# Kernel optimization log

Hardware: AMD Instinct MI355X
Metric: run time of the kernel (lower is better)

The kernel has to match this reference:

```python
import jax, jax.numpy as jnp
import numpy as np

N_EMBD = 1024
N_HEAD = 16
HEAD = N_EMBD // N_HEAD
D_FF = 4 * N_EMBD
B, T = 2, 2048


def setup_inputs() -> dict:
    key = jax.random.key(0)
    ks = jax.random.split(key, 12)
    s = 0.02
    return {
        "x": jax.random.normal(ks[0], (B, T, N_EMBD), jnp.float32),
        "Wq": jax.random.normal(ks[1], (N_EMBD, N_EMBD), jnp.float32) * s,
        "bq": jnp.zeros((N_EMBD,), jnp.float32),
        "Wk": jax.random.normal(ks[2], (N_EMBD, N_EMBD), jnp.float32) * s,
        "bk": jnp.zeros((N_EMBD,), jnp.float32),
        "Wv": jax.random.normal(ks[3], (N_EMBD, N_EMBD), jnp.float32) * s,
        "bv": jnp.zeros((N_EMBD,), jnp.float32),
        "Wo": jax.random.normal(ks[4], (N_EMBD, N_EMBD), jnp.float32) * s,
        "bo": jnp.zeros((N_EMBD,), jnp.float32),
        "W1": jax.random.normal(ks[5], (N_EMBD, D_FF), jnp.float32) * s,
        "b1": jnp.zeros((D_FF,), jnp.float32),
        "W2": jax.random.normal(ks[6], (D_FF, N_EMBD), jnp.float32) * s,
        "b2": jnp.zeros((N_EMBD,), jnp.float32),
        "g1": jnp.ones((N_EMBD,), jnp.float32),
        "be1": jnp.zeros((N_EMBD,), jnp.float32),
        "g2": jnp.ones((N_EMBD,), jnp.float32),
        "be2": jnp.zeros((N_EMBD,), jnp.float32),
    }


def _layernorm(x, g, b, eps=1e-3):
    # keras LayerNormalization default epsilon=1e-3
    mu = jnp.mean(x, axis=-1, keepdims=True)
    var = jnp.mean(jnp.square(x - mu), axis=-1, keepdims=True)
    return (x - mu) * jax.lax.rsqrt(var + eps) * g + b


def _attention(h, Wq, bq, Wk, bk, Wv, bv, Wo, bo):
    b, t, _ = h.shape
    q = (h @ Wq + bq).reshape(b, t, N_HEAD, HEAD)
    k = (h @ Wk + bk).reshape(b, t, N_HEAD, HEAD)
    v = (h @ Wv + bv).reshape(b, t, N_HEAD, HEAD)
    scores = jnp.einsum("bthd,bshd->bhts", q, k) / jnp.sqrt(jnp.float32(HEAD))
    causal = jnp.tril(jnp.ones((t, t), bool))
    scores = jnp.where(causal, scores, -jnp.inf)
    w = jax.nn.softmax(scores, axis=-1)  # dropout is identity in eval
    ctx = jnp.einsum("bhts,bshd->bthd", w, v).reshape(b, t, N_EMBD)
    return ctx @ Wo + bo


def reference(x, Wq, bq, Wk, bk, Wv, bv, Wo, bo, W1, b1, W2, b2, g1, be1, g2, be2):
    x = x + _attention(_layernorm(x, g1, be1), Wq, bq, Wk, bk, Wv, bv, Wo, bo)
    h = _layernorm(x, g2, be2)
    ff = jax.nn.relu(h @ W1 + b1) @ W2 + b2
    return x + ff
```

## Files before the change

### kernel.cpp

```cpp
#include <hip/hip_runtime.h>

typedef __bf16 bf16;
typedef __attribute__((ext_vector_type(8))) __bf16 bf16x8;
typedef __attribute__((ext_vector_type(4))) __bf16 bf16x4;
typedef __attribute__((ext_vector_type(4))) float f32x4;

#define MFMA16(A, B, C) __builtin_amdgcn_mfma_f32_16x16x32_bf16(A, B, C, 0, 0, 0)

#define GLOAD16(gp, lp)                                          \
  __builtin_amdgcn_global_load_lds(                              \
      (const __attribute__((address_space(1))) void*)(gp),       \
      (__attribute__((address_space(3))) void*)(lp), 16, 0, 0)

__device__ __forceinline__ float fexp2(float x) {
#if __has_builtin(__builtin_amdgcn_exp2f)
  return __builtin_amdgcn_exp2f(x);
#else
  float r;
  asm("v_exp_f32 %0, %1" : "=v"(r) : "v"(x));
  return r;
#endif
}

#define QSCL 0.18033688011112042f

__global__ __launch_bounds__(256) void transpose_all_kernel(
    const float* __restrict__ w0, const float* __restrict__ w1,
    const float* __restrict__ w2, const float* __restrict__ w3,
    bf16* __restrict__ out4,
    const float* __restrict__ W1, bf16* __restrict__ w1t,
    const float* __restrict__ W2, bf16* __restrict__ w2t)
{
  __shared__ float tile[32][33];
  const int bid = blockIdx.x;
  const float* in;
  bf16* out;
  int K, N, kt, nt;
  if (bid < 4096) {
    const float* srcs[4] = {w0, w1, w2, w3};
    in = srcs[bid >> 10];
    out = out4 + (size_t)(bid >> 10) * 1024 * 1024;
    K = 1024; N = 1024;
    const int t = bid & 1023;
    nt = (t & 31) * 32; kt = (t >> 5) * 32;
  } else if (bid < 8192) {
    in = W1; out = w1t; K = 1024; N = 4096;
    const int t = bid - 4096;
    nt = (t & 127) * 32; kt = (t >> 7) * 32;
  } else {
    in = W2; out = w2t; K = 4096; N = 1024;
    const int t = bid - 8192;
    nt = (t & 31) * 32; kt = (t >> 5) * 32;
  }
  const int tx = threadIdx.x, ty = threadIdx.y;
#pragma unroll
  for (int j = 0; j < 4; ++j)
    tile[ty + j * 8][tx] = in[(size_t)(kt + ty + j * 8) * N + nt + tx];
  __syncthreads();
#pragma unroll
  for (int j = 0; j < 4; ++j)
    out[(size_t)(nt + ty + j * 8) * K + kt + tx] = (bf16)tile[tx][ty + j * 8];
}

__global__ __launch_bounds__(256) void ln_kernel(
    const float* __restrict__ in, const float* __restrict__ gamma,
    const float* __restrict__ beta, bf16* __restrict__ out)
{
  const int row = blockIdx.x;
  const int t = threadIdx.x;
  const float4 v = ((const float4*)(in + (size_t)row * 1024))[t];
  float s = v.x + v.y + v.z + v.w;
  float sq = v.x * v.x + v.y * v.y + v.z * v.z + v.w * v.w;
#pragma unroll
  for (int m = 1; m < 64; m <<= 1) {
    s += __shfl_xor(s, m);
    sq += __shfl_xor(sq, m);
  }
  __shared__ float ssum[4], ssq[4];
  const int w = t >> 6;
  if ((t & 63) == 0) { ssum[w] = s; ssq[w] = sq; }
  __syncthreads();
  s = ssum[0] + ssum[1] + ssum[2] + ssum[3];
  sq = ssq[0] + ssq[1] + ssq[2] + ssq[3];
  const float mu = s * (1.0f / 1024.0f);
  const float var = sq * (1.0f / 1024.0f) - mu * mu;
  const float rs = rsqrtf(var + 1e-3f);
  const float4 g = ((const float4*)gamma)[t];
  const float4 b = ((const float4*)beta)[t];
  bf16x4 o;
  o[0] = (bf16)((v.x - mu) * rs * g.x + b.x);
  o[1] = (bf16)((v.y - mu) * rs * g.y + b.y);
  o[2] = (bf16)((v.z - mu) * rs * g.z + b.z);
  o[3] = (bf16)((v.w - mu) * rs * g.w + b.w);
  *(bf16x4*)(out + (size_t)row * 1024 + t * 4) = o;
}

__global__ __launch_bounds__(256) void ln_b_kernel(
    const bf16* __restrict__ in, const float* __restrict__ gamma,
    const float* __restrict__ beta, bf16* __restrict__ out)
{
  const int row = blockIdx.x;
  const int t = threadIdx.x;
  const bf16x4 vb = *(const bf16x4*)(in + (size_t)row * 1024 + t * 4);
  float v0 = (float)vb[0], v1 = (float)vb[1], v2 = (float)vb[2], v3 = (float)vb[3];
  float s = v0 + v1 + v2 + v3;
  float sq = v0 * v0 + v1 * v1 + v2 * v2 + v3 * v3;
#pragma unroll
  for (int m = 1; m < 64; m <<= 1) {
    s += __shfl_xor(s, m);
    sq += __shfl_xor(sq, m);
  }
  __shared__ float ssum[4], ssq[4];
  const int w = t >> 6;
  if ((t & 63) == 0) { ssum[w] = s; ssq[w] = sq; }
  __syncthreads();
  s = ssum[0] + ssum[1] + ssum[2] + ssum[3];
  sq = ssq[0] + ssq[1] + ssq[2] + ssq[3];
  const float mu = s * (1.0f / 1024.0f);
  const float var = sq * (1.0f / 1024.0f) - mu * mu;
  const float rs = rsqrtf(var + 1e-3f);
  const float4 g = ((const float4*)gamma)[t];
  const float4 b = ((const float4*)beta)[t];
  bf16x4 o;
  o[0] = (bf16)((v0 - mu) * rs * g.x + b.x);
  o[1] = (bf16)((v1 - mu) * rs * g.y + b.y);
  o[2] = (bf16)((v2 - mu) * rs * g.z + b.z);
  o[3] = (bf16)((v3 - mu) * rs * g.w + b.w);
  *(bf16x4*)(out + (size_t)row * 1024 + t * 4) = o;
}

template <int BM, int BN, int BK, int EPI, int SWZ>
__global__ __launch_bounds__(256, 2) void gemm_bt(
    const bf16* __restrict__ A, const bf16* __restrict__ Bt,
    const float* __restrict__ bias0, const float* __restrict__ bias1,
    const float* __restrict__ bias2, const float* __restrict__ resid,
    const bf16* __restrict__ residb,
    bf16* __restrict__ out0, bf16* __restrict__ out1, bf16* __restrict__ out2,
    float* __restrict__ outf, int M, int N, int K)
{
  constexpr int WM = BM / 2, WN = BN / 2;
  constexpr int MI = WM / 16, NJ = WN / 16;
  constexpr int KK = BK / 32;
  constexpr int NSLOT = BK / 8;
  constexpr int SMASK = NSLOT - 1;
  constexpr int RPL = 512 / BK;
  constexpr int ALOADS = BM / (4 * RPL);
  constexpr int BLOADS = BN / (4 * RPL);
  constexpr int S = ALOADS + BLOADS;

  __shared__ bf16 As[3][BM * BK];
  __shared__ bf16 Bs[3][BN * BK];
  const int tid = threadIdx.x;
  const int lane = tid & 63, w = tid >> 6;
  const int wr = w >> 1, wc = w & 1;
  const int g = lane >> 4, lr = lane & 15;

  int bx = blockIdx.x, by = blockIdx.y;
  if constexpr (SWZ) {
    const int bid = bx + gridDim.x * by;
    const int xcd = bid & 7, idx = bid >> 3;
    const int chunk = gridDim.y >> 3;
    by = xcd * chunk + (idx % chunk);
    bx = idx / chunk;
  }
  const int brow = by * BM, bcol = bx * BN;

  f32x4 acc[MI][NJ] = {};

  const int lrow = lane / NSLOT;
  const int slot = lane & SMASK;
  int lcol;
  if constexpr (BK == 32)
    lcol = ((slot - (lrow >> 1)) & 3) * 8;
  else
    lcol = (slot ^ (lrow & 7)) * 8;

  auto stage = [&](int buf, int k0) {
#pragma unroll
    for (int j = 0; j < ALOADS; ++j) {
      const int row0 = w * (BM / 4) + j * RPL;
      GLOAD16(A + (size_t)(brow + row0 + lrow) * K + k0 + lcol,
              &As[buf][row0 * BK]);
    }
#pragma unroll
    for (int j = 0; j < BLOADS; ++j) {
      const int row0 = w * (BN / 4) + j * RPL;
      GLOAD16(Bt + (size_t)(bcol + row0 + lrow) * K + k0 + lcol,
              &Bs[buf][row0 * BK]);
    }
  };

  auto rdslot = [&](int kg) {
    if constexpr (BK == 32) return ((kg + (lr >> 1)) & 3) * 8;
    else return (kg ^ (lr & 7)) * 8;
  };

  const int nk = K / BK;
  stage(0, 0);
  stage(1, BK);
  int cur = 0;
  for (int t = 0; t < nk; ++t) {
    if (t + 1 < nk) {
      if constexpr (S == 3)
        asm volatile("s_waitcnt vmcnt(3)" ::: "memory");
      else if constexpr (S == 4)
        asm volatile("s_waitcnt vmcnt(4)" ::: "memory");
      else
        asm volatile("s_waitcnt vmcnt(6)" ::: "memory");
    } else {
      asm volatile("s_waitcnt vmcnt(0)" ::: "memory");
    }
    __builtin_amdgcn_s_barrier();
    __builtin_amdgcn_sched_barrier(0);

    bf16x8 afr[MI][KK], bfr[NJ][KK];
#pragma unroll
    for (int i = 0; i < MI; ++i)
#pragma unroll
      for (int kk = 0; kk < KK; ++kk)
        afr[i][kk] = *(const bf16x8*)&As[cur][(wr * WM + i * 16 + lr) * BK +
                                             rdslot(kk * 4 + g)];
#pragma unroll
    for (int j = 0; j < NJ; ++j)
#pragma unroll
      for (int kk = 0; kk < KK; ++kk)
        bfr[j][kk] = *(const bf16x8*)&Bs[cur][(wc * WN + j * 16 + lr) * BK +
                                             rdslot(kk * 4 + g)];

    if (t + 2 < nk) {
      int nb = cur + 2;
      if (nb >= 3) nb -= 3;
      stage(nb, (t + 2) * BK);
    }

    __builtin_amdgcn_s_setprio(1);
#pragma unroll
    for (int kk = 0; kk < KK; ++kk)
#pragma unroll
      for (int i = 0; i < MI; ++i)
#pragma unroll
        for (int j = 0; j < NJ; ++j)
          acc[i][j] = MFMA16(afr[i][kk], bfr[j][kk], acc[i][j]);
    __builtin_amdgcn_s_setprio(0);

    ++cur;
    if (cur == 3) cur = 0;
  }

#pragma unroll
  for (int i = 0; i < MI; ++i) {
#pragma unroll
    for (int j = 0; j < NJ; ++j) {
      const int r0 = brow + wr * WM + i * 16 + g * 4;
      const int c = bcol + wc * WN + j * 16 + lr;
      if constexpr (EPI == 1) {
        const float bv = bias0[c];
#pragma unroll
        for (int rr = 0; rr < 4; ++rr)
          out0[(size_t)(r0 + rr) * N + c] =
              (bf16)fmaxf(acc[i][j][rr] + bv, 0.0f);
      } else if constexpr (EPI == 5) {
        const float bv = bias0[c];
#pragma unroll
        for (int rr = 0; rr < 4; ++rr) {
          const size_t idx = (size_t)(r0 + rr) * N + c;
          out0[idx] = (bf16)(acc[i][j][rr] + bv + resid[idx]);
        }
      } else if constexpr (EPI == 6) {
        const float bv = bias0[c];
#pragma unroll
        for (int rr = 0; rr < 4; ++rr) {
          const size_t idx = (size_t)(r0 + rr) * N + c;
          outf[idx] = acc[i][j][rr] + bv + (float)residb[idx];
        }
      } else {
        const int sub = c >> 10;
        const int c1 = c & 1023;
        if (sub == 0) {
          const float bv = bias0[c1];
#pragma unroll
          for (int rr = 0; rr < 4; ++rr)
            out0[(size_t)(r0 + rr) * 1024 + c1] =
                (bf16)((acc[i][j][rr] + bv) * QSCL);
        } else if (sub == 1) {
          const float bv = bias1[c1];
#pragma unroll
          for (int rr = 0; rr < 4; ++rr)
            out1[(size_t)(r0 + rr) * 1024 + c1] = (bf16)(acc[i][j][rr] + bv);
        } else {
          const float bv = bias2[c1];
          const int bb = r0 >> 11, t0 = r0 & 2047;
          const int hh = c1 >> 6, dd = c1 & 63;
          bf16x4 pk;
#pragma unroll
          for (int rr = 0; rr < 4; ++rr) pk[rr] = (bf16)(acc[i][j][rr] + bv);
          *(bf16x4*)(out2 + ((size_t)((bb * 16 + hh) * 64 + dd)) * 2048 + t0) = pk;
        }
      }
    }
  }
}

__global__ __launch_bounds__(256) void attn_kernel(
    const bf16* __restrict__ q, const bf16* __restrict__ kmat,
    const bf16* __restrict__ vt, bf16* __restrict__ ctx)
{
  __shared__ bf16 Ks[64 * 64];
  __shared__ bf16 Vs[64 * 64];
  __shared__ bf16 Pq[4][16][88];
  const int bx = blockIdx.x, by = blockIdx.y;
  const int k4 = by >> 3;
  const int qt = (k4 == 0) ? bx
               : (k4 == 1) ? (31 - bx)
               : (k4 == 2) ? (bx ^ 16)
                           : (31 - (bx ^ 16));
  const int b_ = by >> 4, h_ = by & 15;
  const int qb = qt * 64;
  const int tid = threadIdx.x;
  const int lane = tid & 63, w = tid >> 6;
  const int g = lane >> 4, lr = lane & 15;
  const int qrow = qb + w * 16 + lr;

  bf16x8 qf[2];
  {
    const bf16* qp = q + (size_t)(b_ * 2048 + qrow) * 1024 + h_ * 64 + g * 8;
    qf[0] = *(const bf16x8*)qp;
    qf[1] = *(const bf16x8*)(qp + 32);
  }

  f32x4 o[4] = {};
  float l = 0.f;

  const int srow = tid >> 2;
  const int c16 = (tid & 3) * 16;
  const int rb = srow * 128;
  const int sw = (srow & 7) << 4;
  const bf16* kbase = kmat + (size_t)(b_ * 2048) * 1024 + h_ * 64;
  const bf16* vbase = vt + (size_t)(b_ * 16 + h_) * 64 * 2048;
  const bf16* kp0 = kbase + (size_t)srow * 1024 + c16;
  const bf16* vp0 = vbase + (size_t)srow * 2048 + c16;

  bf16x8 k0 = *(const bf16x8*)kp0;
  bf16x8 k1 = *(const bf16x8*)(kp0 + 8);
  bf16x8 v0 = *(const bf16x8*)vp0;
  bf16x8 v1 = *(const bf16x8*)(vp0 + 8);

  for (int s0 = 0; s0 <= qb; s0 += 64) {
    *(bf16x8*)((char*)Ks + ((rb + c16 * 2) ^ sw)) = k0;
    *(bf16x8*)((char*)Ks + ((rb + c16 * 2 + 16) ^ sw)) = k1;
    *(bf16x8*)((char*)Vs + ((rb + c16 * 2) ^ sw)) = v0;
    *(bf16x8*)((char*)Vs + ((rb + c16 * 2 + 16) ^ sw)) = v1;
    __syncthreads();
    if (s0 < qb) {
      const bf16* kp = kp0 + (size_t)(s0 + 64) * 1024;
      k0 = *(const bf16x8*)kp;
      k1 = *(const bf16x8*)(kp + 8);
      const bf16* vp = vp0 + (s0 + 64);
      v0 = *(const bf16x8*)vp;
      v1 = *(const bf16x8*)(vp + 8);
    }

    f32x4 st[4];
    __builtin_amdgcn_s_setprio(1);
#pragma unroll
    for (int n = 0; n < 4; ++n) {
      f32x4 z = {};
#pragma unroll
      for (int kk = 0; kk < 2; ++kk) {
        const int row = n * 16 + lr;
        bf16x8 ak = *(const bf16x8*)((char*)Ks +
            ((row * 128 + kk * 64 + g * 16) ^ ((lr & 7) << 4)));
        z = MFMA16(ak, qf[kk], z);
      }
      st[n] = z;
    }
    __builtin_amdgcn_s_setprio(0);

    if (s0 == qb) {
#pragma unroll
      for (int n = 0; n < 4; ++n)
#pragma unroll
        for (int r = 0; r < 4; ++r)
          if (s0 + n * 16 + g * 4 + r > qrow) st[n][r] = -1e30f;
    }

    float rs = 0.f;
#pragma unroll
    for (int n = 0; n < 4; ++n) {
      bf16x4 pk;
#pragma unroll
      for (int r = 0; r < 4; ++r) {
        const float p = fexp2(st[n][r]);
        rs += p;
        pk[r] = (bf16)p;
      }
      *(bf16x4*)&Pq[w][lr][n * 16 + g * 4] = pk;
    }

    bf16x8 pa[2];
#pragma unroll
    for (int kk = 0; kk < 2; ++kk)
      pa[kk] = *(const bf16x8*)&Pq[w][lr][kk * 32 + g * 8];
    __builtin_amdgcn_s_setprio(1);
#pragma unroll
    for (int n = 0; n < 4; ++n) {
      const int row = n * 16 + lr;
#pragma unroll
      for (int kk = 0; kk < 2; ++kk) {
        bf16x8 bv = *(const bf16x8*)((char*)Vs +
            ((row * 128 + kk * 64 + g * 16) ^ ((lr & 7) << 4)));
        o[n] = MFMA16(pa[kk], bv, o[n]);
      }
    }
    __builtin_amdgcn_s_setprio(0);

    rs += __shfl_xor(rs, 16);
    rs += __shfl_xor(rs, 32);
    l += rs;
    __syncthreads();
  }

  float lq[4];
#pragma unroll
  for (int r = 0; r < 4; ++r) lq[r] = __shfl(l, g * 4 + r);
#pragma unroll
  for (int r = 0; r < 4; ++r) {
    const float inv = 1.0f / lq[r];
#pragma unroll
    for (int n = 0; n < 4; ++n)
      ctx[(size_t)(b_ * 2048 + qb + w * 16 + g * 4 + r) * 1024 + h_ * 64 + n * 16 + lr] =
          (bf16)(o[n][r] * inv);
  }
}

extern "C" void kernel_launch(void* const* d_in, const int* in_sizes, int n_in,
                              void* d_out, int out_size, void* d_ws, size_t ws_size,
                              hipStream_t stream)
{
  (void)in_sizes; (void)n_in; (void)out_size; (void)ws_size;
  const float* x   = (const float*)d_in[0];
  const float* Wq  = (const float*)d_in[1];
  const float* bq  = (const float*)d_in[2];
  const float* Wk  = (const float*)d_in[3];
  const float* bk  = (const float*)d_in[4];
  const float* Wv  = (const float*)d_in[5];
  const float* bv  = (const float*)d_in[6];
  const float* Wo  = (const float*)d_in[7];
  const float* bo  = (const float*)d_in[8];
  const float* W1  = (const float*)d_in[9];
  const float* b1  = (const float*)d_in[10];
  const float* W2  = (const float*)d_in[11];
  const float* b2  = (const float*)d_in[12];
  const float* g1  = (const float*)d_in[13];
  const float* be1 = (const float*)d_in[14];
  const float* g2  = (const float*)d_in[15];
  const float* be2 = (const float*)d_in[16];
  float* out = (float*)d_out;

  char* ws = (char*)d_ws;
  const size_t MB = 1024 * 1024;
  bf16* wqkv_t = (bf16*)(ws + 0 * MB);
  bf16* wo_t = (bf16*)(ws + 6 * MB);
  bf16* w1_t = (bf16*)(ws + 8 * MB);
  bf16* w2_t = (bf16*)(ws + 16 * MB);
  bf16* h1   = (bf16*)(ws + 24 * MB);
  bf16* qbuf = (bf16*)(ws + 32 * MB);
  bf16* kbuf = (bf16*)(ws + 40 * MB);
  bf16* vtb  = (bf16*)(ws + 48 * MB);
  bf16* ctx  = (bf16*)(ws + 56 * MB);
  bf16* h2   = (bf16*)(ws + 64 * MB);
  bf16* x2b  = (bf16*)(ws + 72 * MB);
  bf16* ff1  = (bf16*)(ws + 24 * MB);

  transpose_all_kernel<<<12288, dim3(32, 8), 0, stream>>>(
      Wq, Wk, Wv, Wo, wqkv_t, W1, w1_t, W2, w2_t);

  ln_kernel<<<4096, 256, 0, stream>>>(x, g1, be1, h1);

  gemm_bt<128, 128, 32, 4, 0><<<dim3(24, 32), 256, 0, stream>>>(
      h1, wqkv_t, bq, bk, bv, nullptr, nullptr, qbuf, kbuf, vtb, nullptr,
      4096, 3072, 1024);

  attn_kernel<<<dim3(32, 32), 256, 0, stream>>>(qbuf, kbuf, vtb, ctx);

  gemm_bt<128, 64, 64, 5, 0><<<dim3(16, 32), 256, 0, stream>>>(
      ctx, wo_t, bo, nullptr, nullptr, x, nullptr, x2b, nullptr, nullptr,
      nullptr, 4096, 1024, 1024);

  ln_b_kernel<<<4096, 256, 0, stream>>>(x2b, g2, be2, h2);

  gemm_bt<256, 128, 32, 1, 0><<<dim3(32, 16), 256, 0, stream>>>(
      h2, w1_t, b1, nullptr, nullptr, nullptr, nullptr, ff1, nullptr, nullptr,
      nullptr, 4096, 4096, 1024);

  gemm_bt<128, 64, 64, 6, 1><<<dim3(16, 32), 256, 0, stream>>>(
      ff1, w2_t, b2, nullptr, nullptr, nullptr, x2b, nullptr, nullptr, nullptr,
      out, 4096, 1024, 4096);
}
```

Measured before the change: 198.6 us.

## Load attention K/V fragments directly from global per wave, drop LDS staging

The attention kernel no longer stages K and V tiles through shared memory with block-wide barriers. Each wave now loads its K and V MFMA fragments straight from global memory. Each wave also owns an independent 16-row query tile, chosen so the four waves of a block get complementary causal workloads. This removes the LDS round trip and the per-iteration __syncthreads. In exchange, K/V reuse across the four waves of a block is lost, which raises global/L2 traffic and exposes load latency without explicit prefetching.

```diff
diff --git a/kernel.cpp b/kernel.cpp
--- a/kernel.cpp
+++ b/kernel.cpp
@@ -305,21 +305,20 @@
     const bf16* __restrict__ q, const bf16* __restrict__ kmat,
     const bf16* __restrict__ vt, bf16* __restrict__ ctx)
 {
-  __shared__ bf16 Ks[64 * 64];
-  __shared__ bf16 Vs[64 * 64];
   __shared__ bf16 Pq[4][16][88];
-  const int bx = blockIdx.x, by = blockIdx.y;
-  const int k4 = by >> 3;
-  const int qt = (k4 == 0) ? bx
-               : (k4 == 1) ? (31 - bx)
-               : (k4 == 2) ? (bx ^ 16)
-                           : (31 - (bx ^ 16));
-  const int b_ = by >> 4, h_ = by & 15;
-  const int qb = qt * 64;
+  const int bid = blockIdx.x;
+  const int a = bid >> 5;
+  const int bh = bid & 31;
+  const int b_ = bh >> 4, h_ = bh & 15;
   const int tid = threadIdx.x;
   const int lane = tid & 63, w = tid >> 6;
   const int g = lane >> 4, lr = lane & 15;
-  const int qrow = qb + w * 16 + lr;
+
+  const int p = (w + (bid >> 8)) & 3;
+  const int qt16 = (p == 0) ? a : (p == 1) ? (127 - a)
+                 : (p == 2) ? (63 - a) : (64 + a);
+  const int q0 = qt16 * 16;
+  const int qrow = q0 + lr;
 
   bf16x8 qf[2];
   {
@@ -331,33 +330,19 @@
   f32x4 o[4] = {};
   float l = 0.f;
 
-  const int srow = tid >> 2;
-  const int c16 = (tid & 3) * 16;
-  const int rb = srow * 128;
-  const int sw = (srow & 7) << 4;
   const bf16* kbase = kmat + (size_t)(b_ * 2048) * 1024 + h_ * 64;
   const bf16* vbase = vt + (size_t)(b_ * 16 + h_) * 64 * 2048;
-  const bf16* kp0 = kbase + (size_t)srow * 1024 + c16;
-  const bf16* vp0 = vbase + (size_t)srow * 2048 + c16;
-
-  bf16x8 k0 = *(const bf16x8*)kp0;
-  bf16x8 k1 = *(const bf16x8*)(kp0 + 8);
-  bf16x8 v0 = *(const bf16x8*)vp0;
-  bf16x8 v1 = *(const bf16x8*)(vp0 + 8);
-
-  for (int s0 = 0; s0 <= qb; s0 += 64) {
-    *(bf16x8*)((char*)Ks + ((rb + c16 * 2) ^ sw)) = k0;
-    *(bf16x8*)((char*)Ks + ((rb + c16 * 2 + 16) ^ sw)) = k1;
-    *(bf16x8*)((char*)Vs + ((rb + c16 * 2) ^ sw)) = v0;
-    *(bf16x8*)((char*)Vs + ((rb + c16 * 2 + 16) ^ sw)) = v1;
-    __syncthreads();
-    if (s0 < qb) {
-      const bf16* kp = kp0 + (size_t)(s0 + 64) * 1024;
-      k0 = *(const bf16x8*)kp;
-      k1 = *(const bf16x8*)(kp + 8);
-      const bf16* vp = vp0 + (s0 + 64);
-      v0 = *(const bf16x8*)vp;
-      v1 = *(const bf16x8*)(vp + 8);
+
+  const int ns = (qt16 >> 2) + 1;
+  for (int t = 0; t < ns; ++t) {
+    const int s0 = t << 6;
+
+    bf16x8 ak[4][2];
+#pragma unroll
+    for (int n = 0; n < 4; ++n) {
+      const bf16* kp = kbase + (size_t)(s0 + n * 16 + lr) * 1024 + g * 8;
+      ak[n][0] = *(const bf16x8*)kp;
+      ak[n][1] = *(const bf16x8*)(kp + 32);
     }
 
     f32x4 st[4];
@@ -365,18 +350,21 @@
 #pragma unroll
     for (int n = 0; n < 4; ++n) {
       f32x4 z = {};
-#pragma unroll
-      for (int kk = 0; kk < 2; ++kk) {
-        const int row = n * 16 + lr;
-        bf16x8 ak = *(const bf16x8*)((char*)Ks +
-            ((row * 128 + kk * 64 + g * 16) ^ ((lr & 7) << 4)));
-        z = MFMA16(ak, qf[kk], z);
-      }
+      z = MFMA16(ak[n][0], qf[0], z);
+      z = MFMA16(ak[n][1], qf[1], z);
       st[n] = z;
     }
     __builtin_amdgcn_s_setprio(0);
 
-    if (s0 == qb) {
+    bf16x8 bv[4][2];
+#pragma unroll
+    for (int n = 0; n < 4; ++n) {
+      const bf16* vp = vbase + (size_t)(n * 16 + lr) * 2048 + s0 + g * 8;
+      bv[n][0] = *(const bf16x8*)vp;
+      bv[n][1] = *(const bf16x8*)(vp + 32);
+    }
+
+    if (t == ns - 1) {
 #pragma unroll
       for (int n = 0; n < 4; ++n)
 #pragma unroll
@@ -390,9 +378,9 @@
       bf16x4 pk;
 #pragma unroll
       for (int r = 0; r < 4; ++r) {
-        const float p = fexp2(st[n][r]);
-        rs += p;
-        pk[r] = (bf16)p;
+        const float pv = fexp2(st[n][r]);
+        rs += pv;
+        pk[r] = (bf16)pv;
       }
       *(bf16x4*)&Pq[w][lr][n * 16 + g * 4] = pk;
     }
@@ -404,20 +392,14 @@
     __builtin_amdgcn_s_setprio(1);
 #pragma unroll
     for (int n = 0; n < 4; ++n) {
-      const int row = n * 16 + lr;
-#pragma unroll
-      for (int kk = 0; kk < 2; ++kk) {
-        bf16x8 bv = *(const bf16x8*)((char*)Vs +
-            ((row * 128 + kk * 64 + g * 16) ^ ((lr & 7) << 4)));
-        o[n] = MFMA16(pa[kk], bv, o[n]);
-      }
+      o[n] = MFMA16(pa[0], bv[n][0], o[n]);
+      o[n] = MFMA16(pa[1], bv[n][1], o[n]);
     }
     __builtin_amdgcn_s_setprio(0);
 
     rs += __shfl_xor(rs, 16);
     rs += __shfl_xor(rs, 32);
     l += rs;
-    __syncthreads();
   }
 
   float lq[4];
@@ -428,7 +410,7 @@
     const float inv = 1.0f / lq[r];
 #pragma unroll
     for (int n = 0; n < 4; ++n)
-      ctx[(size_t)(b_ * 2048 + qb + w * 16 + g * 4 + r) * 1024 + h_ * 64 + n * 16 + lr] =
+      ctx[(size_t)(b_ * 2048 + q0 + g * 4 + r) * 1024 + h_ * 64 + n * 16 + lr] =
           (bf16)(o[n][r] * inv);
   }
 }
@@ -481,7 +463,7 @@
       h1, wqkv_t, bq, bk, bv, nullptr, nullptr, qbuf, kbuf, vtb, nullptr,
       4096, 3072, 1024);
 
-  attn_kernel<<<dim3(32, 32), 256, 0, stream>>>(qbuf, kbuf, vtb, ctx);
+  attn_kernel<<<1024, 256, 0, stream>>>(qbuf, kbuf, vtb, ctx);
 
   gemm_bt<128, 64, 64, 5, 0><<<dim3(16, 32), 256, 0, stream>>>(
       ctx, wo_t, bo, nullptr, nullptr, x, nullptr, x2b, nullptr, nullptr,
```

New measurement: 276.9 us. +39.5%, slower.
